# Kernel optimization log

Hardware: AMD Instinct MI355X
Metric: run time of the kernel (lower is better)

## Reference

```python
import jax, jax.numpy as jnp
import numpy as np

B, L = 64, 8192
WIN = 3            # unfold window size
H = 90             # surrogate MLP hidden width (brains-py default)
N_ELEC = 7         # total electrodes; data on 2,3,4; controls on 0,1,5,6
AMP = 28.5         # electrode_effects amplification


def setup_inputs() -> dict:
    key = jax.random.key(0)
    ks = jax.random.split(key, 16)
    x = jax.random.normal(ks[0], (B, L), dtype=jnp.float32)
    # 4 learned control voltages (electrodes 0,1,5,6), plausible voltage range
    cv = jax.random.uniform(ks[1], (4,), dtype=jnp.float32, minval=-1.2, maxval=0.6)
    def lin(k, fan_in, fan_out):
        w = jax.random.normal(k, (fan_in, fan_out), dtype=jnp.float32) * np.sqrt(2.0 / fan_in).astype(np.float32)
        return w
    W1 = lin(ks[2], N_ELEC, H); b1 = jnp.zeros((H,), jnp.float32)
    W2 = lin(ks[3], H, H);      b2 = jnp.zeros((H,), jnp.float32)
    W3 = lin(ks[4], H, H);      b3 = jnp.zeros((H,), jnp.float32)
    W4 = lin(ks[5], H, H);      b4 = jnp.zeros((H,), jnp.float32)
    W5 = lin(ks[6], H, H);      b5 = jnp.zeros((H,), jnp.float32)
    W6 = lin(ks[7], H, 1);      b6 = jnp.zeros((1,), jnp.float32)
    return {"x": x, "cv": cv,
            "W1": W1, "b1": b1, "W2": W2, "b2": b2, "W3": W3, "b3": b3,
            "W4": W4, "b4": b4, "W5": W5, "b5": b5, "W6": W6, "b6": b6}


def reference(x, cv, W1, b1, W2, b2, W3, b3, W4, b4, W5, b5, W6, b6):
    Bq, Lq = x.shape
    n_win = Lq - WIN + 1
    # sliding windows (unfold(1, 3, 1)): [B, n_win, 3]
    idx = jnp.arange(n_win)[:, None] + jnp.arange(WIN)[None, :]
    win = x[:, idx]  # [B, n_win, 3]
    # assemble 7-electrode input: cv[0:2] | data window | cv[2:4]
    cv_lo = jnp.broadcast_to(cv[:2], (Bq, n_win, 2))
    cv_hi = jnp.broadcast_to(cv[2:], (Bq, n_win, 2))
    z = jnp.concatenate([cv_lo, win, cv_hi], axis=-1)  # [B, n_win, 7]
    h = jax.nn.relu(z @ W1 + b1)
    h = jax.nn.relu(h @ W2 + b2)
    h = jax.nn.relu(h @ W3 + b3)
    h = jax.nn.relu(h @ W4 + b4)
    h = jax.nn.relu(h @ W5 + b5)
    out = (h @ W6 + b6) * AMP  # [B, n_win, 1]
    return out[..., 0]  # squeeze -> [B, n_win]
```

## Files before the change

### kernel.cpp

```cpp
#include <hip/hip_runtime.h>

#define NB   64
#define LSEQ 8192
#define NW   8190
#define HD   90
#define AMPF 28.5f
#define NTILE 4

typedef _Float16 half8  __attribute__((ext_vector_type(8)));
typedef float    f32x16 __attribute__((ext_vector_type(16)));
typedef __fp16   fp16x2 __attribute__((ext_vector_type(2)));

union FragU { uint4 u; half8 h; };

__device__ __forceinline__ unsigned pk2(float a, float b) {
  fp16x2 v = __builtin_amdgcn_cvt_pkrtz(a, b);
  return __builtin_bit_cast(unsigned, v);
}
__device__ __forceinline__ unsigned pkmax0(unsigned w) {
  unsigned r;
  asm("v_pk_max_f16 %0, %1, %2" : "=v"(r) : "v"(w), "v"(0u));
  return r;
}

__global__ void dnpu_pack(const float* __restrict__ W1, const float* __restrict__ b1,
                          const float* __restrict__ W2, const float* __restrict__ b2,
                          const float* __restrict__ W3, const float* __restrict__ b3,
                          const float* __restrict__ W4, const float* __restrict__ b4,
                          const float* __restrict__ W5, const float* __restrict__ b5,
                          const float* __restrict__ W6, const float* __restrict__ b6,
                          uint4* __restrict__ frags) {
  int tid = blockIdx.x * blockDim.x + threadIdx.x;
  if (tid >= 81 * 64) return;
  int f = tid >> 6, lane = tid & 63;
  int n = lane & 31, g = lane >> 5;
  const float* W; const float* bias; int t2, ks, kin, nout;
  if (f < 3) {
    W = W1; bias = b1; t2 = f; ks = 0; kin = 7; nout = HD;
  } else if (f < 75) {
    int q = f - 3; int L = q / 18; int r = q % 18;
    t2 = r / 6; ks = r % 6; kin = HD; nout = HD;
    W    = (L == 0) ? W2 : (L == 1) ? W3 : (L == 2) ? W4 : W5;
    bias = (L == 0) ? b2 : (L == 1) ? b3 : (L == 2) ? b4 : b5;
  } else {
    W = W6; bias = b6; t2 = 0; ks = f - 75; kin = HD; nout = 1;
  }
  int row = 32 * t2 + n;
  FragU u;
#pragma unroll
  for (int i = 0; i < 8; ++i) {
    int k = 16 * ks + 8 * g + i;
    float val = 0.f;
    if (row < nout) {
      if (k < kin)       val = W[k * nout + row];
      else if (k == kin) val = bias[row];
    }
    if (row == HD && k == kin && f < 75) val = 1.0f;
    u.h[i] = (_Float16)val;
  }
  frags[f * 64 + lane] = u.u;
}

__device__ __forceinline__ void transition(const f32x16 (&acc)[3], uint4 (&Bt)[6]) {
  unsigned P0[3][4], P1[3][4];
#pragma unroll
  for (int u = 0; u < 3; ++u) {
#pragma unroll
    for (int q = 0; q < 4; ++q) {
      P0[u][q] = pkmax0(pk2(acc[u][4 * q + 0], acc[u][4 * q + 1]));
      P1[u][q] = pkmax0(pk2(acc[u][4 * q + 2], acc[u][4 * q + 3]));
    }
  }
#pragma unroll
  for (int u = 0; u < 3; ++u) {
#pragma unroll
    for (int par = 0; par < 2; ++par) {
      unsigned w0 = P0[u][2 * par], w2 = P0[u][2 * par + 1];
      unsigned w1 = P1[u][2 * par], w3 = P1[u][2 * par + 1];
      asm("v_permlane32_swap_b32 %0, %1" : "+v"(w0), "+v"(w2));
      asm("v_permlane32_swap_b32 %0, %1" : "+v"(w1), "+v"(w3));
      Bt[2 * u + par] = make_uint4(w0, w1, w2, w3);
    }
  }
}

__global__ __launch_bounds__(256, 2)
void dnpu_mfma(const float* __restrict__ x, const float* __restrict__ cv,
               const uint4* __restrict__ frags, float* __restrict__ out) {
  __shared__ uint4 lfr[36 * 64];
  const int tid  = threadIdx.x;
  const int lane = tid & 63, wid = tid >> 6;
  const int g = lane >> 5, c = lane & 31;
  const int b = blockIdx.y;

  for (int i = tid; i < 36 * 64; i += 256) lfr[i] = frags[192 + i];
  __syncthreads();

  const float c0 = cv[0], c1 = cv[1], c2 = cv[2], c3 = cv[3];
  const float* xr = x + (size_t)b * LSEQ;
  const int rowbase0 = blockIdx.x * 512 + wid * 128;

  uint4 Bw[NTILE][6];

  {
    FragU Af[3];
#pragma unroll
    for (int t2 = 0; t2 < 3; ++t2) Af[t2].u = frags[t2 * 64 + lane];
#pragma unroll
    for (int t = 0; t < NTILE; ++t) {
      const int w  = rowbase0 + t * 32 + c;
      const int xi = (w < LSEQ - 3) ? w : (LSEQ - 3);
      const float x0 = xr[xi], x1 = xr[xi + 1], x2 = xr[xi + 2];
      half8 B1;
#pragma unroll
      for (int i = 0; i < 8; ++i) B1[i] = (_Float16)0.f;
      if (g == 0) {
        B1[0] = (_Float16)c0; B1[1] = (_Float16)c1;
        B1[2] = (_Float16)x0; B1[3] = (_Float16)x1; B1[4] = (_Float16)x2;
        B1[5] = (_Float16)c2; B1[6] = (_Float16)c3; B1[7] = (_Float16)1.0f;
      }
      f32x16 acc[3];
#pragma unroll
      for (int t2 = 0; t2 < 3; ++t2)
        acc[t2] = __builtin_amdgcn_mfma_f32_32x32x16_f16(Af[t2].h, B1, (f32x16)(0.f), 0, 0, 0);
      transition(acc, Bw[t]);
    }
  }

#pragma unroll 1
  for (int L = 0; L < 4; ++L) {
    FragU Af[18];
    if (L < 2) {
#pragma unroll
      for (int j = 0; j < 18; ++j) Af[j].u = lfr[(L * 18 + j) * 64 + lane];
    } else {
#pragma unroll
      for (int j = 0; j < 18; ++j) Af[j].u = frags[(3 + L * 18 + j) * 64 + lane];
    }
#pragma unroll
    for (int t = 0; t < NTILE; ++t) {
      f32x16 acc[3];
#pragma unroll
      for (int t2 = 0; t2 < 3; ++t2) {
        f32x16 a = (f32x16)(0.f);
#pragma unroll
        for (int ks = 0; ks < 6; ++ks)
          a = __builtin_amdgcn_mfma_f32_32x32x16_f16(
                Af[t2 * 6 + ks].h, __builtin_bit_cast(half8, Bw[t][ks]), a, 0, 0, 0);
        acc[t2] = a;
      }
      transition(acc, Bw[t]);
    }
  }

  {
    FragU Af[6];
#pragma unroll
    for (int ks = 0; ks < 6; ++ks) Af[ks].u = frags[(75 + ks) * 64 + lane];
#pragma unroll
    for (int t = 0; t < NTILE; ++t) {
      f32x16 a = (f32x16)(0.f);
#pragma unroll
      for (int ks = 0; ks < 6; ++ks)
        a = __builtin_amdgcn_mfma_f32_32x32x16_f16(
              Af[ks].h, __builtin_bit_cast(half8, Bw[t][ks]), a, 0, 0, 0);
      if (g == 0) {
        const int row = rowbase0 + t * 32 + c;
        if (row < NW) out[(size_t)b * NW + row] = a[0] * AMPF;
      }
    }
  }
}

extern "C" void kernel_launch(void* const* d_in, const int* in_sizes, int n_in,
                              void* d_out, int out_size, void* d_ws, size_t ws_size,
                              hipStream_t stream) {
  const float* x  = (const float*)d_in[0];
  const float* cv = (const float*)d_in[1];
  const float* W1 = (const float*)d_in[2];
  const float* b1 = (const float*)d_in[3];
  const float* W2 = (const float*)d_in[4];
  const float* b2 = (const float*)d_in[5];
  const float* W3 = (const float*)d_in[6];
  const float* b3 = (const float*)d_in[7];
  const float* W4 = (const float*)d_in[8];
  const float* b4 = (const float*)d_in[9];
  const float* W5 = (const float*)d_in[10];
  const float* b5 = (const float*)d_in[11];
  const float* W6 = (const float*)d_in[12];
  const float* b6 = (const float*)d_in[13];
  float* out = (float*)d_out;
  uint4* frags = (uint4*)d_ws;

  hipLaunchKernelGGL(dnpu_pack, dim3(21), dim3(256), 0, stream,
                     W1, b1, W2, b2, W3, b3, W4, b4, W5, b5, W6, b6, frags);
  hipLaunchKernelGGL(dnpu_mfma, dim3(16, NB), dim3(256), 0, stream,
                     x, cv, frags, out);
}
```

Measured before the change: 53.34 us.

## Halve per-wave tiles and stream weights from LDS per MFMA to cut registers

Each wave now handles two 32-row tiles instead of four, and the grid is doubled so the same rows are still covered. Weight fragments are no longer held in an 18-register array. They are loaded from LDS per MFMA, with all four hidden layers staged through two LDS buffers that are refilled between layers behind barriers. The aim is lower register pressure and more blocks in flight. The cost is extra LDS traffic, four extra block-wide barriers and reloading weights per tile.

```diff
diff --git a/kernel.cpp b/kernel.cpp
--- a/kernel.cpp
+++ b/kernel.cpp
@@ -5,7 +5,7 @@
 #define NW   8190
 #define HD   90
 #define AMPF 28.5f
-#define NTILE 4
+#define NTILE 2
 
 typedef _Float16 half8  __attribute__((ext_vector_type(8)));
 typedef float    f32x16 __attribute__((ext_vector_type(16)));
@@ -84,90 +84,92 @@
   }
 }
 
+__device__ __forceinline__ void hidden_layer(const uint4* __restrict__ src, int lane,
+                                             uint4 (&Bw)[NTILE][6]) {
+#pragma unroll
+  for (int t = 0; t < NTILE; ++t) {
+    f32x16 acc[3];
+#pragma unroll
+    for (int u = 0; u < 3; ++u) {
+      f32x16 a = (f32x16)(0.f);
+#pragma unroll
+      for (int ks = 0; ks < 6; ++ks) {
+        FragU Af; Af.u = src[(u * 6 + ks) * 64 + lane];
+        a = __builtin_amdgcn_mfma_f32_32x32x16_f16(
+              Af.h, __builtin_bit_cast(half8, Bw[t][ks]), a, 0, 0, 0);
+      }
+      acc[u] = a;
+    }
+    transition(acc, Bw[t]);
+  }
+}
+
 __global__ __launch_bounds__(256, 2)
 void dnpu_mfma(const float* __restrict__ x, const float* __restrict__ cv,
                const uint4* __restrict__ frags, float* __restrict__ out) {
-  __shared__ uint4 lfr[36 * 64];
+  __shared__ uint4 lfr[2][18 * 64];
   const int tid  = threadIdx.x;
   const int lane = tid & 63, wid = tid >> 6;
   const int g = lane >> 5, c = lane & 31;
   const int b = blockIdx.y;
 
-  for (int i = tid; i < 36 * 64; i += 256) lfr[i] = frags[192 + i];
+  for (int i = tid; i < 18 * 64; i += 256) {
+    lfr[0][i] = frags[3 * 64 + i];
+    lfr[1][i] = frags[21 * 64 + i];
+  }
   __syncthreads();
 
   const float c0 = cv[0], c1 = cv[1], c2 = cv[2], c3 = cv[3];
   const float* xr = x + (size_t)b * LSEQ;
-  const int rowbase0 = blockIdx.x * 512 + wid * 128;
+  const int rowbase0 = blockIdx.x * (NTILE * 32 * 4) + wid * (NTILE * 32);
 
   uint4 Bw[NTILE][6];
 
-  {
-    FragU Af[3];
-#pragma unroll
-    for (int t2 = 0; t2 < 3; ++t2) Af[t2].u = frags[t2 * 64 + lane];
-#pragma unroll
-    for (int t = 0; t < NTILE; ++t) {
-      const int w  = rowbase0 + t * 32 + c;
-      const int xi = (w < LSEQ - 3) ? w : (LSEQ - 3);
-      const float x0 = xr[xi], x1 = xr[xi + 1], x2 = xr[xi + 2];
-      half8 B1;
-#pragma unroll
-      for (int i = 0; i < 8; ++i) B1[i] = (_Float16)0.f;
-      if (g == 0) {
-        B1[0] = (_Float16)c0; B1[1] = (_Float16)c1;
-        B1[2] = (_Float16)x0; B1[3] = (_Float16)x1; B1[4] = (_Float16)x2;
-        B1[5] = (_Float16)c2; B1[6] = (_Float16)c3; B1[7] = (_Float16)1.0f;
-      }
-      f32x16 acc[3];
-#pragma unroll
-      for (int t2 = 0; t2 < 3; ++t2)
-        acc[t2] = __builtin_amdgcn_mfma_f32_32x32x16_f16(Af[t2].h, B1, (f32x16)(0.f), 0, 0, 0);
-      transition(acc, Bw[t]);
-    }
-  }
-
-#pragma unroll 1
-  for (int L = 0; L < 4; ++L) {
-    FragU Af[18];
-    if (L < 2) {
-#pragma unroll
-      for (int j = 0; j < 18; ++j) Af[j].u = lfr[(L * 18 + j) * 64 + lane];
-    } else {
-#pragma unroll
-      for (int j = 0; j < 18; ++j) Af[j].u = frags[(3 + L * 18 + j) * 64 + lane];
-    }
-#pragma unroll
-    for (int t = 0; t < NTILE; ++t) {
-      f32x16 acc[3];
-#pragma unroll
-      for (int t2 = 0; t2 < 3; ++t2) {
-        f32x16 a = (f32x16)(0.f);
-#pragma unroll
-        for (int ks = 0; ks < 6; ++ks)
-          a = __builtin_amdgcn_mfma_f32_32x32x16_f16(
-                Af[t2 * 6 + ks].h, __builtin_bit_cast(half8, Bw[t][ks]), a, 0, 0, 0);
-        acc[t2] = a;
-      }
-      transition(acc, Bw[t]);
-    }
-  }
-
-  {
-    FragU Af[6];
-#pragma unroll
-    for (int ks = 0; ks < 6; ++ks) Af[ks].u = frags[(75 + ks) * 64 + lane];
-#pragma unroll
-    for (int t = 0; t < NTILE; ++t) {
-      f32x16 a = (f32x16)(0.f);
-#pragma unroll
-      for (int ks = 0; ks < 6; ++ks)
-        a = __builtin_amdgcn_mfma_f32_32x32x16_f16(
-              Af[ks].h, __builtin_bit_cast(half8, Bw[t][ks]), a, 0, 0, 0);
-      if (g == 0) {
-        const int row = rowbase0 + t * 32 + c;
-        if (row < NW) out[(size_t)b * NW + row] = a[0] * AMPF;
-      }
+#pragma unroll
+  for (int t = 0; t < NTILE; ++t) {
+    const int w  = rowbase0 + t * 32 + c;
+    const int xi = (w < LSEQ - 3) ? w : (LSEQ - 3);
+    const float x0 = xr[xi], x1 = xr[xi + 1], x2 = xr[xi + 2];
+    half8 B1;
+#pragma unroll
+    for (int i = 0; i < 8; ++i) B1[i] = (_Float16)0.f;
+    if (g == 0) {
+      B1[0] = (_Float16)c0; B1[1] = (_Float16)c1;
+      B1[2] = (_Float16)x0; B1[3] = (_Float16)x1; B1[4] = (_Float16)x2;
+      B1[5] = (_Float16)c2; B1[6] = (_Float16)c3; B1[7] = (_Float16)1.0f;
+    }
+    f32x16 acc[3];
+#pragma unroll
+    for (int t2 = 0; t2 < 3; ++t2) {
+      FragU Af; Af.u = frags[t2 * 64 + lane];
+      acc[t2] = __builtin_amdgcn_mfma_f32_32x32x16_f16(Af.h, B1, (f32x16)(0.f), 0, 0, 0);
+    }
+    transition(acc, Bw[t]);
+  }
+
+  hidden_layer(&lfr[0][0], lane, Bw);
+  __syncthreads();
+  for (int i = tid; i < 18 * 64; i += 256) lfr[0][i] = frags[39 * 64 + i];
+  __syncthreads();
+  hidden_layer(&lfr[1][0], lane, Bw);
+  __syncthreads();
+  for (int i = tid; i < 18 * 64; i += 256) lfr[1][i] = frags[57 * 64 + i];
+  __syncthreads();
+  hidden_layer(&lfr[0][0], lane, Bw);
+  hidden_layer(&lfr[1][0], lane, Bw);
+
+#pragma unroll
+  for (int t = 0; t < NTILE; ++t) {
+    f32x16 a = (f32x16)(0.f);
+#pragma unroll
+    for (int ks = 0; ks < 6; ++ks) {
+      FragU Af; Af.u = frags[(75 + ks) * 64 + lane];
+      a = __builtin_amdgcn_mfma_f32_32x32x16_f16(
+            Af.h, __builtin_bit_cast(half8, Bw[t][ks]), a, 0, 0, 0);
+    }
+    if (g == 0) {
+      const int row = rowbase0 + t * 32 + c;
+      if (row < NW) out[(size_t)b * NW + row] = a[0] * AMPF;
     }
   }
 }
@@ -194,6 +196,6 @@
 
   hipLaunchKernelGGL(dnpu_pack, dim3(21), dim3(256), 0, stream,
                      W1, b1, W2, b2, W3, b3, W4, b4, W5, b5, W6, b6, frags);
-  hipLaunchKernelGGL(dnpu_mfma, dim3(16, NB), dim3(256), 0, stream,
+  hipLaunchKernelGGL(dnpu_mfma, dim3(32, NB), dim3(256), 0, stream,
                      x, cv, frags, out);
 }
```

Result: faster. 48.51 us (-9.1%).
